# Performance work log

Hardware: AMD Instinct MI355X
Metric: run time of the kernel (lower is better)

Reference implementation:

```python
import jax, jax.numpy as jnp
import numpy as np

N, C, H, W = 16, 64, 256, 256
M_BUCKETS = 128  # min(H*W/144, 128) saturates at 128 for H=W=256


def setup_inputs() -> dict:
    key = jax.random.key(0)
    k1, k2 = jax.random.split(key)
    inputs = jax.random.normal(k1, (N, C, H, W), dtype=jnp.float32)
    # LSH random-projection matrices, one per batch element: (N, C, m)
    random_matrices = jax.random.normal(k2, (N, C, M_BUCKETS), dtype=jnp.float32)
    return {"inputs": inputs, "random_matrices": random_matrices}


def reference(inputs, random_matrices):
    n, c, h, w = inputs.shape
    # Flatten spatial dims: each of the H*W pixels has a C-dim feature vector.
    x = inputs.reshape(n, c, h * w)  # (N, C, P) with P = H*W
    # Per-pixel hash logits via random projection: (N, P, m)
    hash_code = jnp.einsum('ncp,ncm->npm', x, random_matrices)
    return hash_code
```

## Files before the change

### kernel.cpp

```cpp
#include <hip/hip_runtime.h>


#define NB   16
#define CDIM 64
#define PDIM 65536
#define MDIM 128
#define PT   128
#define NWIN 512
#define WSTRIDE 80
#define XS   132

typedef __attribute__((ext_vector_type(8))) short bf16x8;
typedef __attribute__((ext_vector_type(4))) float f32x4;

__device__ __forceinline__ unsigned short f2bf(float f) {
  union { float f; unsigned int u; } v; v.f = f;
  unsigned int u = v.u;
  u += 0x7fffu + ((u >> 16) & 1u);
  return (unsigned short)(u >> 16);
}

__device__ __forceinline__ unsigned int pack2bf(float flo, float fhi) {
  union { float f; unsigned int u; } a, b;
  a.f = flo; b.f = fhi;
  unsigned int ua = a.u + (0x7fffu + ((a.u >> 16) & 1u));
  unsigned int ub = b.u + (0x7fffu + ((b.u >> 16) & 1u));
  return (ua >> 16) | (ub & 0xffff0000u);
}

union pk8 { bf16x8 f; unsigned int u[4]; };

__device__ __forceinline__ int xswz(int c, int p) {
  return c * XS + (p ^ (((c >> 3) & 3) << 4));
}

__global__ __launch_bounds__(256, 5) void nlsa_kernel(
    const float* __restrict__ x, const float* __restrict__ rm,
    float* __restrict__ out) {
  __shared__ unsigned short lds_x[CDIM * XS];

  const int t = threadIdx.x;
  const int b = blockIdx.x;
  const int n  = b & 15;
  const int w0 = b >> 4;

  const float* xn   = x  + (size_t)n * CDIM * PDIM;
  const float* rmn  = rm + (size_t)n * CDIM * MDIM;
  float*       outn = out + (size_t)n * PDIM * MDIM;

  const int cst = t >> 5;
  const int pst = (t & 31) * 4;

  float4 r[8];
  {
    const float* src = xn + (size_t)(w0 * PT + pst);
#pragma unroll
    for (int it = 0; it < 8; ++it)
      r[it] = *(const float4*)(src + (size_t)(cst + it * 8) * PDIM);
  }

  const int w_ = t >> 6;
  const int l  = t & 63;
  const int lo = l & 15;
  const int g  = l >> 4;

  bf16x8 a[2][2];
  {
    const float* rs = rmn + (size_t)(g * 8) * MDIM + w_ * 32 + lo;
#pragma unroll
    for (int mt = 0; mt < 2; ++mt)
#pragma unroll
      for (int ks = 0; ks < 2; ++ks) {
        float v[8];
#pragma unroll
        for (int i = 0; i < 8; ++i)
          v[i] = rs[(size_t)(ks * 32 + i) * MDIM + mt * 16];
        pk8 p;
#pragma unroll
        for (int j = 0; j < 4; ++j) p.u[j] = pack2bf(v[2 * j], v[2 * j + 1]);
        a[mt][ks] = p.f;
      }
  }

  for (int w = w0; w < NWIN; w += WSTRIDE) {
    asm volatile("" ::: "memory");
    __builtin_amdgcn_s_barrier();
    asm volatile("" ::: "memory");

#pragma unroll
    for (int it = 0; it < 8; ++it) {
      ushort4 v;
      v.x = f2bf(r[it].x); v.y = f2bf(r[it].y);
      v.z = f2bf(r[it].z); v.w = f2bf(r[it].w);
      *(ushort4*)&lds_x[xswz(cst + it * 8, pst)] = v;
    }

    if (w + WSTRIDE < NWIN) {
      const float* src = xn + (size_t)((w + WSTRIDE) * PT + pst);
#pragma unroll
      for (int it = 0; it < 8; ++it)
        r[it] = *(const float4*)(src + (size_t)(cst + it * 8) * PDIM);
    }

    asm volatile("s_waitcnt lgkmcnt(0)" ::: "memory");
    __builtin_amdgcn_s_barrier();
    asm volatile("" ::: "memory");

    const int p_base = w * PT;
#pragma unroll
    for (int pt_ = 0; pt_ < 8; ++pt_) {
      const int pl  = pt_ * 16 + lo;
      const int pls = pl ^ (g << 4);
      bf16x8 b0, b1;
#pragma unroll
      for (int i = 0; i < 8; ++i) {
        b0[i] = (short)lds_x[(g * 8 + i) * XS + pls];
        b1[i] = (short)lds_x[(32 + g * 8 + i) * XS + pls];
      }
      f32x4 acc0 = {0.f, 0.f, 0.f, 0.f};
      f32x4 acc1 = {0.f, 0.f, 0.f, 0.f};
      acc0 = __builtin_amdgcn_mfma_f32_16x16x32_bf16(a[0][0], b0, acc0, 0, 0, 0);
      acc0 = __builtin_amdgcn_mfma_f32_16x16x32_bf16(a[0][1], b1, acc0, 0, 0, 0);
      acc1 = __builtin_amdgcn_mfma_f32_16x16x32_bf16(a[1][0], b0, acc1, 0, 0, 0);
      acc1 = __builtin_amdgcn_mfma_f32_16x16x32_bf16(a[1][1], b1, acc1, 0, 0, 0);

      float* dst = outn + (size_t)(p_base + pl) * MDIM + w_ * 32 + g * 4;
      *(f32x4*)(dst)      = acc0;
      *(f32x4*)(dst + 16) = acc1;
    }
  }
}

extern "C" void kernel_launch(void* const* d_in, const int* in_sizes, int n_in,
                              void* d_out, int out_size, void* d_ws, size_t ws_size,
                              hipStream_t stream) {
  const float* x  = (const float*)d_in[0];
  const float* rm = (const float*)d_in[1];
  float* out = (float*)d_out;
  nlsa_kernel<<<dim3(NB * WSTRIDE), dim3(256), 0, stream>>>(x, rm, out);
}
```

Before: 177.1 us.

## Load input tiles directly into LDS as fp32 and convert to bf16 at read

Replaces the register-staged load, bf16 conversion and swizzled LDS store with direct global-to-LDS loads (global_load_lds, 16 bytes per lane) of fp32 tiles. The bf16 packing now happens when each wave reads its B operands from LDS. The register prefetch of the next window is dropped, so the load and compute of successive windows no longer overlap within a block. LDS per block doubles (32 KB), which may limit occupancy, and the unswizzled fp32 reads may cause bank conflicts.

```diff
diff --git a/kernel.cpp b/kernel.cpp
--- a/kernel.cpp
+++ b/kernel.cpp
@@ -8,7 +8,7 @@
 #define PT   128
 #define NWIN 512
 #define WSTRIDE 80
-#define XS   132
+#define GRID (NB * WSTRIDE)
 
 typedef __attribute__((ext_vector_type(8))) short bf16x8;
 typedef __attribute__((ext_vector_type(4))) float f32x4;
@@ -30,14 +30,10 @@
 
 union pk8 { bf16x8 f; unsigned int u[4]; };
 
-__device__ __forceinline__ int xswz(int c, int p) {
-  return c * XS + (p ^ (((c >> 3) & 3) << 4));
-}
-
 __global__ __launch_bounds__(256, 5) void nlsa_kernel(
     const float* __restrict__ x, const float* __restrict__ rm,
     float* __restrict__ out) {
-  __shared__ unsigned short lds_x[CDIM * XS];
+  __shared__ float lds_xf[CDIM * PT];
 
   const int t = threadIdx.x;
   const int b = blockIdx.x;
@@ -47,17 +43,6 @@
   const float* xn   = x  + (size_t)n * CDIM * PDIM;
   const float* rmn  = rm + (size_t)n * CDIM * MDIM;
   float*       outn = out + (size_t)n * PDIM * MDIM;
-
-  const int cst = t >> 5;
-  const int pst = (t & 31) * 4;
-
-  float4 r[8];
-  {
-    const float* src = xn + (size_t)(w0 * PT + pst);
-#pragma unroll
-    for (int it = 0; it < 8; ++it)
-      r[it] = *(const float4*)(src + (size_t)(cst + it * 8) * PDIM);
-  }
 
   const int w_ = t >> 6;
   const int l  = t & 63;
@@ -82,49 +67,49 @@
       }
   }
 
+  const size_t lane_off = (size_t)(l >> 5) * PDIM + (l & 31) * 4;
+
   for (int w = w0; w < NWIN; w += WSTRIDE) {
     asm volatile("" ::: "memory");
     __builtin_amdgcn_s_barrier();
     asm volatile("" ::: "memory");
 
+    {
+      const float* gbase = xn + (size_t)w * PT + lane_off;
 #pragma unroll
-    for (int it = 0; it < 8; ++it) {
-      ushort4 v;
-      v.x = f2bf(r[it].x); v.y = f2bf(r[it].y);
-      v.z = f2bf(r[it].z); v.w = f2bf(r[it].w);
-      *(ushort4*)&lds_x[xswz(cst + it * 8, pst)] = v;
+      for (int i = 0; i < 8; ++i) {
+        const int c0 = 16 * w_ + 2 * i;
+        const float* gp = gbase + (size_t)c0 * PDIM;
+        float* lp = &lds_xf[c0 * PT];
+        __builtin_amdgcn_global_load_lds(
+            (const __attribute__((address_space(1))) unsigned int*)gp,
+            (__attribute__((address_space(3))) unsigned int*)lp, 16, 0, 0);
+      }
     }
-
-    if (w + WSTRIDE < NWIN) {
-      const float* src = xn + (size_t)((w + WSTRIDE) * PT + pst);
-#pragma unroll
-      for (int it = 0; it < 8; ++it)
-        r[it] = *(const float4*)(src + (size_t)(cst + it * 8) * PDIM);
-    }
-
-    asm volatile("s_waitcnt lgkmcnt(0)" ::: "memory");
+    asm volatile("s_waitcnt vmcnt(0)" ::: "memory");
     __builtin_amdgcn_s_barrier();
     asm volatile("" ::: "memory");
 
     const int p_base = w * PT;
 #pragma unroll
     for (int pt_ = 0; pt_ < 8; ++pt_) {
-      const int pl  = pt_ * 16 + lo;
-      const int pls = pl ^ (g << 4);
-      bf16x8 b0, b1;
+      const int prow = pt_ * 16 + lo;
+      pk8 b0, b1;
 #pragma unroll
-      for (int i = 0; i < 8; ++i) {
-        b0[i] = (short)lds_x[(g * 8 + i) * XS + pls];
-        b1[i] = (short)lds_x[(32 + g * 8 + i) * XS + pls];
+      for (int j = 0; j < 4; ++j) {
+        b0.u[j] = pack2bf(lds_xf[(g * 8 + 2 * j) * PT + prow],
+                          lds_xf[(g * 8 + 2 * j + 1) * PT + prow]);
+        b1.u[j] = pack2bf(lds_xf[(32 + g * 8 + 2 * j) * PT + prow],
+                          lds_xf[(32 + g * 8 + 2 * j + 1) * PT + prow]);
       }
       f32x4 acc0 = {0.f, 0.f, 0.f, 0.f};
       f32x4 acc1 = {0.f, 0.f, 0.f, 0.f};
-      acc0 = __builtin_amdgcn_mfma_f32_16x16x32_bf16(a[0][0], b0, acc0, 0, 0, 0);
-      acc0 = __builtin_amdgcn_mfma_f32_16x16x32_bf16(a[0][1], b1, acc0, 0, 0, 0);
-      acc1 = __builtin_amdgcn_mfma_f32_16x16x32_bf16(a[1][0], b0, acc1, 0, 0, 0);
-      acc1 = __builtin_amdgcn_mfma_f32_16x16x32_bf16(a[1][1], b1, acc1, 0, 0, 0);
+      acc0 = __builtin_amdgcn_mfma_f32_16x16x32_bf16(a[0][0], b0.f, acc0, 0, 0, 0);
+      acc0 = __builtin_amdgcn_mfma_f32_16x16x32_bf16(a[0][1], b1.f, acc0, 0, 0, 0);
+      acc1 = __builtin_amdgcn_mfma_f32_16x16x32_bf16(a[1][0], b0.f, acc1, 0, 0, 0);
+      acc1 = __builtin_amdgcn_mfma_f32_16x16x32_bf16(a[1][1], b1.f, acc1, 0, 0, 0);
 
-      float* dst = outn + (size_t)(p_base + pl) * MDIM + w_ * 32 + g * 4;
+      float* dst = outn + (size_t)(p_base + prow) * MDIM + w_ * 32 + g * 4;
       *(f32x4*)(dst)      = acc0;
       *(f32x4*)(dst + 16) = acc1;
     }
@@ -137,5 +122,5 @@
   const float* x  = (const float*)d_in[0];
   const float* rm = (const float*)d_in[1];
   float* out = (float*)d_out;
-  nlsa_kernel<<<dim3(NB * WSTRIDE), dim3(256), 0, stream>>>(x, rm, out);
+  nlsa_kernel<<<dim3(GRID), dim3(256), 0, stream>>>(x, rm, out);
 }
```

New measurement: 182.3 us. 1.03x slower.
